# Performance work log

Hardware: AMD Instinct MI355X
Metric: run time of the kernel (lower is better)

Reference implementation:

```python
import jax, jax.numpy as jnp
import numpy as np

HEADS = 6
EPS = 1e-5


def _na_idx(L, k, d):
    # NATTEN-style dilated neighborhood: work within dilation cosets,
    # clamp window to stay inside the image (window shifts at borders).
    i = np.arange(L)
    g = i % d
    p = i // d
    Lg = (L - g + d - 1) // d  # coset length per position
    start = np.clip(p - k // 2, 0, Lg - k)
    j = np.arange(k)
    nbr = g[:, None] + d * (start[:, None] + j[None, :])          # [L,k] neighbor coords
    rel = (start[:, None] + j[None, :]) - p[:, None] + (k - 1)    # [L,k] rpb index in [0,2k-2]
    return jnp.asarray(nbr, jnp.int32), jnp.asarray(rel, jnp.int32)


def _na2d(x, qkv_w, qkv_b, proj_w, proj_b, rpb, heads, k, d):
    # x: [B,H,W,C] NHWC neighborhood attention with relative positional bias
    B, H, W, C = x.shape
    dh = C // heads
    scale = dh ** -0.5
    qkv = (x @ qkv_w + qkv_b).reshape(B, H, W, 3, heads, dh)
    qkv = jnp.transpose(qkv, (3, 0, 4, 1, 2, 5))  # [3,B,h,H,W,dh]
    q, kk, v = qkv[0] * scale, qkv[1], qkv[2]
    nh, rh = _na_idx(H, k, d)
    nw, rw = _na_idx(W, k, d)

    def gather(t):  # [B,h,H,W,dh] -> [B,h,H,W,k,k,dh]
        t = t[:, :, nh]              # [B,h,H,k,W,dh]
        t = t[:, :, :, :, nw]        # [B,h,H,k,W,k,dh]
        return jnp.transpose(t, (0, 1, 2, 4, 3, 5, 6))

    kn, vn = gather(kk), gather(v)
    attn = jnp.einsum('bhxyd,bhxyijd->bhxyij', q, kn)  # [B,h,H,W,k,k]
    bias = rpb[:, rh]                  # [h,H,k,2k-1]
    bias = bias[:, :, :, rw]           # [h,H,k,W,k]
    bias = jnp.transpose(bias, (0, 1, 3, 2, 4))  # [h,H,W,k,k]
    attn = attn + bias[None]
    attn = jax.nn.softmax(attn.reshape(B, heads, H, W, k * k), axis=-1)
    attn = attn.reshape(B, heads, H, W, k, k)
    out = jnp.einsum('bhxyij,bhxyijd->bhxyd', attn, vn)
    out = jnp.transpose(out, (0, 2, 3, 1, 4)).reshape(B, H, W, C)
    return out @ proj_w + proj_b


def _rln(x, w, b, m1_w, m1_b, m2_w, m2_b):
    # Revised LayerNorm: normalize over (C,H,W) per sample; meta1/meta2 are 1x1 convs on std/mean
    mean = jnp.mean(x, axis=(1, 2, 3), keepdims=True)
    std = jnp.sqrt(jnp.mean((x - mean) ** 2, axis=(1, 2, 3), keepdims=True) + EPS)
    out = (x - mean) / std * w + b
    rescale = m1_w[None, :, None, None] * std + m1_b[None, :, None, None]
    rebias = m2_w[None, :, None, None] * mean + m2_b[None, :, None, None]
    return out, rescale, rebias


def _c11(x, w, b):  # 1x1 conv on NCHW == per-pixel linear
    return jnp.einsum('bchw,oc->bohw', x, w) + b[None, :, None, None]


def _gelu(x):
    return jax.nn.gelu(x, approximate=False)


def reference(x, ln_w, ln_b, m1_w, m1_b, m2_w, m2_b, qkv1_w, qkv1_b, proj1_w, proj1_b, rpb1, qkv2_w, qkv2_b, proj2_w, proj2_b, rpb2, mlp_w1, mlp_b1, mlp_w2, mlp_b2, bn_g, bn_b, bn_m, bn_v, pa_w1, pa_b1, pa_w2, pa_b2, ca_w1, ca_b1, ca_w2, ca_b2, m2a_w1, m2a_b1, m2a_w2, m2a_b2):
    # ---- NA block 1 (kernel 7, dilation 1) ----
    sc = x
    y, rs, rb = _rln(x, ln_w, ln_b, m1_w, m1_b, m2_w, m2_b)
    a = _na2d(jnp.transpose(y, (0, 2, 3, 1)), qkv1_w, qkv1_b, proj1_w, proj1_b, rpb1, HEADS, 7, 1)
    x = sc + jnp.transpose(a, (0, 3, 1, 2)) * rs + rb
    # ---- NA block 2 (kernel 5, dilation 8) ----
    sc = x
    y, rs, rb = _rln(x, ln_w, ln_b, m1_w, m1_b, m2_w, m2_b)
    a = _na2d(jnp.transpose(y, (0, 2, 3, 1)), qkv2_w, qkv2_b, proj2_w, proj2_b, rpb2, HEADS, 5, 8)
    x = sc + jnp.transpose(a, (0, 3, 1, 2)) * rs + rb
    # ---- MLP (source reuses the pre-attn2 shortcut `sc`) ----
    y, rs, rb = _rln(x, ln_w, ln_b, m1_w, m1_b, m2_w, m2_b)
    m = _c11(jax.nn.relu(_c11(y, mlp_w1, mlp_b1)), mlp_w2, mlp_b2)
    x = sc + m * rs + rb
    # ---- BN + pixel attention + channel attention + mlp2 ----
    sc = x
    inv = jax.lax.rsqrt(bn_v + EPS)
    y = (x - bn_m[None, :, None, None]) * (inv * bn_g)[None, :, None, None] + bn_b[None, :, None, None]
    pa = jax.nn.sigmoid(_c11(_gelu(_c11(y, pa_w1, pa_b1)), pa_w2, pa_b2))  # [B,1,H,W]
    y = pa * y
    gap = jnp.mean(y, axis=(2, 3), keepdims=True)
    ca = jax.nn.sigmoid(_c11(_gelu(_c11(gap, ca_w1, ca_b1)), ca_w2, ca_b2))  # [B,C,1,1]
    y = ca * y
    y = _c11(_gelu(_c11(y, m2a_w1, m2a_b1)), m2a_w2, m2a_b2)
    return sc + y


def setup_inputs() -> dict:
    key = jax.random.key(0)
    B, C, H, W, HID = 4, 96, 64, 64, 384
    ks = iter(jax.random.split(key, 48))

    def rn(shape, s=0.02):
        return jax.random.normal(next(ks), shape, jnp.float32) * s

    d = {}
    d['x'] = jax.random.normal(next(ks), (B, C, H, W), jnp.float32)
    d['ln_w'] = jnp.ones((1, C, 1, 1), jnp.float32)
    d['ln_b'] = jnp.zeros((1, C, 1, 1), jnp.float32)
    d['m1_w'] = rn((C,)); d['m1_b'] = jnp.ones((C,), jnp.float32)
    d['m2_w'] = rn((C,)); d['m2_b'] = jnp.zeros((C,), jnp.float32)
    d['qkv1_w'] = rn((C, 3 * C)); d['qkv1_b'] = jnp.zeros((3 * C,), jnp.float32)
    d['proj1_w'] = rn((C, C)); d['proj1_b'] = jnp.zeros((C,), jnp.float32)
    d['rpb1'] = rn((HEADS, 13, 13))
    d['qkv2_w'] = rn((C, 3 * C)); d['qkv2_b'] = jnp.zeros((3 * C,), jnp.float32)
    d['proj2_w'] = rn((C, C)); d['proj2_b'] = jnp.zeros((C,), jnp.float32)
    d['rpb2'] = rn((HEADS, 9, 9))
    d['mlp_w1'] = rn((HID, C)); d['mlp_b1'] = jnp.zeros((HID,), jnp.float32)
    d['mlp_w2'] = rn((C, HID)); d['mlp_b2'] = jnp.zeros((C,), jnp.float32)
    d['bn_g'] = jnp.ones((C,), jnp.float32); d['bn_b'] = jnp.zeros((C,), jnp.float32)
    d['bn_m'] = jnp.zeros((C,), jnp.float32); d['bn_v'] = jnp.ones((C,), jnp.float32)
    d['pa_w1'] = rn((C // 8, C)); d['pa_b1'] = jnp.zeros((C // 8,), jnp.float32)
    d['pa_w2'] = rn((1, C // 8)); d['pa_b2'] = jnp.zeros((1,), jnp.float32)
    d['ca_w1'] = rn((C, C)); d['ca_b1'] = jnp.zeros((C,), jnp.float32)
    d['ca_w2'] = rn((C, C)); d['ca_b2'] = jnp.zeros((C,), jnp.float32)
    d['m2a_w1'] = rn((C, C)); d['m2a_b1'] = jnp.zeros((C,), jnp.float32)
    d['m2a_w2'] = rn((C, C)); d['m2a_b2'] = jnp.zeros((C,), jnp.float32)
    return d
```

## Files before the change

kernel.cpp:

```cpp
#include <hip/hip_runtime.h>
#include <math.h>

#define CC 96
#define NP 4096
#define NHEADS 6
#define NELEMF 393216.0f
#define EPSF 1e-5f

typedef __attribute__((ext_vector_type(8))) short bf16x8;
typedef __attribute__((ext_vector_type(4))) float f32x4;
#define MFMA16(a,b,c) __builtin_amdgcn_mfma_f32_16x16x32_bf16(a,b,c,0,0,0)

#define WQKV1  64
#define WQKV2  (WQKV1+13824)
#define WPROJ1 (WQKV2+13824)
#define WPROJ2 (WPROJ1+4608)
#define WMLP1  (WPROJ2+4608)
#define WMLP2  (WMLP1+18432)
#define WM2A1  (WMLP2+18432)
#define WM2A2  (WM2A1+4608)
#define WPA1T  (WM2A2+4608)
#define WBNS   (WPA1T+1152)
#define WS_Q   870784
#define WS_K   (WS_Q+786432)
#define WS_V   (WS_K+786432)
#define WS_ATTPM (WS_V+786432)
#define WS_X1  (WS_ATTPM+786432)
#define WS_X2  (WS_X1+1572864)
#define WS_X3  (WS_X2+1572864)
#define WS_PA  (WS_X3+1572864)
#define WS_GAP (WS_PA+16384)
#define WS_CA  (WS_GAP+384)

__device__ __forceinline__ float gelu_f(float x){
  return 0.5f * x * (1.0f + erff(x * 0.7071067811865476f));
}
__device__ __forceinline__ float sigmoid_f(float x){
  return 1.0f / (1.0f + __expf(-x));
}
__device__ __forceinline__ unsigned short bfr(float f){
  unsigned int u = __float_as_uint(f);
  u += 0x7fffu + ((u >> 16) & 1u);
  return (unsigned short)(u >> 16);
}
__device__ __forceinline__ float bflo(unsigned int u){ return __uint_as_float(u << 16); }
__device__ __forceinline__ float bfhi(unsigned int u){ return __uint_as_float(u & 0xffff0000u); }
__device__ __forceinline__ void get_ms(const float* st, int b, float& mean, float& inv, float& stdv){
  float s = st[b], s2 = st[4+b];
  mean = s * (1.0f/NELEMF);
  float var = fmaxf(s2 * (1.0f/NELEMF) - mean*mean, 0.0f);
  stdv = sqrtf(var + EPSF);
  inv = 1.0f / stdv;
}

__global__ void prep_stats_kernel(const float* __restrict__ x, float* __restrict__ st,
                             const float* __restrict__ q1, const float* __restrict__ q2,
                             const float* __restrict__ p1, const float* __restrict__ p2,
                             const float* __restrict__ w1, const float* __restrict__ w2,
                             const float* __restrict__ a1, const float* __restrict__ a2,
                             const float* __restrict__ pw1,
                             const float* __restrict__ bg, const float* __restrict__ bb,
                             const float* __restrict__ bm, const float* __restrict__ bv,
                             float* __restrict__ ws){
  if(blockIdx.x < 384){
    int b = blockIdx.x / CC, c = blockIdx.x % CC;
    const float* p = x + (b*CC + c)*NP;
    float s = 0.f, s2 = 0.f;
    for(int i = threadIdx.x; i < NP; i += 256){ float v = p[i]; s += v; s2 = fmaf(v, v, s2); }
    for(int off = 32; off > 0; off >>= 1){ s += __shfl_down(s, off); s2 += __shfl_down(s2, off); }
    __shared__ float ls[8];
    int wid = threadIdx.x >> 6;
    if((threadIdx.x & 63) == 0){ ls[wid] = s; ls[4+wid] = s2; }
    __syncthreads();
    if(threadIdx.x == 0){
      atomicAdd(&st[b],   ls[0]+ls[1]+ls[2]+ls[3]);
      atomicAdd(&st[4+b], ls[4]+ls[5]+ls[6]+ls[7]);
    }
    return;
  }
  int gid = (blockIdx.x - 384)*256 + threadIdx.x;
  if(gid < 27648){ int n = gid/96, c = gid%96; ((unsigned short*)(ws+WQKV1))[gid] = bfr(q1[c*288+n]); }
  else if(gid < 55296){ int g = gid-27648; int n = g/96, c = g%96; ((unsigned short*)(ws+WQKV2))[g] = bfr(q2[c*288+n]); }
  else if(gid < 64512){ int g = gid-55296; int n = g/96, c = g%96; ((unsigned short*)(ws+WPROJ1))[g] = bfr(p1[c*96+n]); }
  else if(gid < 73728){ int g = gid-64512; int n = g/96, c = g%96; ((unsigned short*)(ws+WPROJ2))[g] = bfr(p2[c*96+n]); }
  else if(gid < 110592){ int g = gid-73728; ((unsigned short*)(ws+WMLP1))[g] = bfr(w1[g]); }
  else if(gid < 147456){ int g = gid-110592; ((unsigned short*)(ws+WMLP2))[g] = bfr(w2[g]); }
  else if(gid < 156672){ int g = gid-147456; ((unsigned short*)(ws+WM2A1))[g] = bfr(a1[g]); }
  else if(gid < 165888){ int g = gid-156672; ((unsigned short*)(ws+WM2A2))[g] = bfr(a2[g]); }
  else if(gid < 167040){ int g = gid-165888; int c = g/12, h = g%12; ws[WPA1T + g] = pw1[h*96+c]; }
  else if(gid < 167136){ int c = gid-167040;
    float sc = rsqrtf(bv[c] + EPSF) * bg[c];
    ws[WBNS + c] = sc;
    ws[WBNS + 96 + c] = bb[c] - bm[c]*sc;
  }
}

__global__ void __launch_bounds__(256) gemm_qkv_kernel(
    const float* __restrict__ xin, const float* __restrict__ st,
    const float* __restrict__ lnw, const float* __restrict__ lnb,
    const unsigned short* __restrict__ wT, const float* __restrict__ qb,
    unsigned short* __restrict__ qo, unsigned short* __restrict__ ko, unsigned short* __restrict__ vo){
  __shared__ unsigned short Atl[64*104];
  __shared__ float scl[96], ofs[96];
  int m_base = blockIdx.x*64;
  int nh = blockIdx.y;
  int b = m_base >> 12, pxl0 = m_base & 4095;
  float mean, inv, stdv; get_ms(st, b, mean, inv, stdv);
  int tid = threadIdx.x;
  if(tid < 96){ float s = inv*lnw[tid]; scl[tid] = s; ofs[tid] = lnb[tid] - mean*s; }
  __syncthreads();
  const float* src = xin + (size_t)b*CC*NP + pxl0;
  for(int idx = tid; idx < 96*64; idx += 256){
    int c = idx >> 6, p = idx & 63;
    Atl[p*104 + c] = bfr(fmaf(src[c*NP + p], scl[c], ofs[c]));
  }
  __syncthreads();
  int w = tid >> 6, lane = tid & 63, ml = lane & 15, q = lane >> 4;
  const unsigned short* arow = Atl + (w*16 + ml)*104;
  bf16x8 av[3];
  #pragma unroll
  for(int ks = 0; ks < 3; ++ks) av[ks] = *(const bf16x8*)(arow + ks*32 + q*8);
  f32x4 z = {0.f,0.f,0.f,0.f};
  #pragma unroll
  for(int g = 0; g < 3; ++g){
    f32x4 acc[3] = {z, z, z};
    #pragma unroll
    for(int ks = 0; ks < 3; ++ks){
      #pragma unroll
      for(int gg = 0; gg < 3; ++gg){
        bf16x8 bv = *(const bf16x8*)(wT + (nh*144 + g*48 + gg*16 + ml)*96 + ks*32 + q*8);
        acc[gg] = MFMA16(av[ks], bv, acc[gg]);
      }
    }
    #pragma unroll
    for(int gg = 0; gg < 3; ++gg){
      int nfb = nh*144 + g*48 + gg*16;
      int t = nfb/96, head = (nfb%96) >> 4;
      float scale = (t == 0) ? 0.25f : 1.0f;
      unsigned short* dst = (t == 0) ? qo : (t == 1) ? ko : vo;
      float bias = qb[nfb + ml];
      #pragma unroll
      for(int r = 0; r < 4; ++r){
        int pxl = pxl0 + w*16 + q*4 + r;
        dst[(((size_t)(b*NHEADS + head))*NP + pxl)*16 + ml] = bfr((acc[gg][r] + bias)*scale);
      }
    }
  }
}

__global__ void __launch_bounds__(256) gemm_proj_kernel(
    const unsigned short* __restrict__ attpm, const unsigned short* __restrict__ wT,
    const float* __restrict__ pb, const float* __restrict__ scx, const float* __restrict__ st,
    const float* __restrict__ m1w, const float* __restrict__ m1b,
    const float* __restrict__ m2w, const float* __restrict__ m2b,
    float* __restrict__ dst, float* __restrict__ st_out){
  int w = threadIdx.x >> 6, lane = threadIdx.x & 63;
  int ml = lane & 15, q = lane >> 4;
  int m_base = blockIdx.x*128 + w*32;
  int n0 = blockIdx.y*48;
  f32x4 acc[2][3];
  f32x4 z = {0.f,0.f,0.f,0.f};
  #pragma unroll
  for(int f=0; f<2; ++f) for(int g=0; g<3; ++g) acc[f][g] = z;
  {
    const bf16x8* a0 = (const bf16x8*)(attpm + (size_t)(m_base + ml)*96 + q*8);
    const bf16x8* a1 = (const bf16x8*)(attpm + (size_t)(m_base + 16 + ml)*96 + q*8);
    #pragma unroll
    for(int ks = 0; ks < 3; ++ks){
      bf16x8 av0 = a0[ks*4], av1 = a1[ks*4];
      #pragma unroll
      for(int g = 0; g < 3; ++g){
        bf16x8 bv = *(const bf16x8*)(wT + (n0 + g*16 + ml)*96 + ks*32 + q*8);
        acc[0][g] = MFMA16(av0, bv, acc[0][g]);
        acc[1][g] = MFMA16(av1, bv, acc[1][g]);
      }
    }
  }
  __shared__ float T[48*133];
  #pragma unroll
  for(int f = 0; f < 2; ++f)
    #pragma unroll
    for(int g = 0; g < 3; ++g)
      #pragma unroll
      for(int r = 0; r < 4; ++r)
        T[(g*16 + ml)*133 + w*32 + f*16 + q*4 + r] = acc[f][g][r];
  __syncthreads();
  int b = (blockIdx.x*128) >> 12, pxl0 = (blockIdx.x*128) & 4095;
  float mean, inv, stdv; get_ms(st, b, mean, inv, stdv);
  float s = 0.f, s2 = 0.f;
  for(int idx = threadIdx.x; idx < 48*128; idx += 256){
    int row = idx >> 7, px = idx & 127;
    int n = n0 + row;
    float rsf = fmaf(m1w[n], stdv, m1b[n]);
    float rbf = fmaf(m2w[n], mean, m2b[n]);
    int ad = (b*CC + n)*NP + pxl0 + px;
    float val = scx[ad] + (T[row*133 + px] + pb[n])*rsf + rbf;
    dst[ad] = val;
    s += val; s2 = fmaf(val, val, s2);
  }
  for(int off = 32; off > 0; off >>= 1){ s += __shfl_down(s, off); s2 += __shfl_down(s2, off); }
  __shared__ float ls[8];
  int wid = threadIdx.x >> 6;
  if((threadIdx.x & 63) == 0){ ls[wid] = s; ls[4+wid] = s2; }
  __syncthreads();
  if(threadIdx.x == 0){
    atomicAdd(&st_out[b],   ls[0]+ls[1]+ls[2]+ls[3]);
    atomicAdd(&st_out[4+b], ls[4]+ls[5]+ls[6]+ls[7]);
  }
}

__global__ void __launch_bounds__(256) gemm_mlp1_kernel(
    const float* __restrict__ xin, const float* __restrict__ st,
    const float* __restrict__ lnw, const float* __restrict__ lnb,
    const unsigned short* __restrict__ wT, const float* __restrict__ b1,
    unsigned short* __restrict__ hid){
  __shared__ unsigned short Atl[64*104];
  __shared__ float scl[96], ofs[96];
  int m_base = blockIdx.x*64;
  int nh = blockIdx.y;
  int b = m_base >> 12, pxl0 = m_base & 4095;
  float mean, inv, stdv; get_ms(st, b, mean, inv, stdv);
  int tid = threadIdx.x;
  if(tid < 96){ float s = inv*lnw[tid]; scl[tid] = s; ofs[tid] = lnb[tid] - mean*s; }
  __syncthreads();
  const float* src = xin + (size_t)b*CC*NP + pxl0;
  for(int idx = tid; idx < 96*64; idx += 256){
    int c = idx >> 6, p = idx & 63;
    Atl[p*104 + c] = bfr(fmaf(src[c*NP + p], scl[c], ofs[c]));
  }
  __syncthreads();
  int w = tid >> 6, lane = tid & 63, ml = lane & 15, q = lane >> 4;
  const unsigned short* arow = Atl + (w*16 + ml)*104;
  bf16x8 av[3];
  #pragma unroll
  for(int ks = 0; ks < 3; ++ks) av[ks] = *(const bf16x8*)(arow + ks*32 + q*8);
  f32x4 z = {0.f,0.f,0.f,0.f};
  #pragma unroll
  for(int g = 0; g < 4; ++g){
    f32x4 acc[3] = {z, z, z};
    #pragma unroll
    for(int ks = 0; ks < 3; ++ks){
      #pragma unroll
      for(int gg = 0; gg < 3; ++gg){
        bf16x8 bv = *(const bf16x8*)(wT + (nh*192 + g*48 + gg*16 + ml)*96 + ks*32 + q*8);
        acc[gg] = MFMA16(av[ks], bv, acc[gg]);
      }
    }
    #pragma unroll
    for(int gg = 0; gg < 3; ++gg){
      int n = nh*192 + g*48 + gg*16 + ml;
      float bias = b1[n];
      #pragma unroll
      for(int r = 0; r < 4; ++r){
        int m = m_base + w*16 + q*4 + r;
        hid[(size_t)m*384 + n] = bfr(fmaxf(acc[gg][r] + bias, 0.f));
      }
    }
  }
}

__global__ void __launch_bounds__(256) gemm_mlp2_kernel(
    const unsigned short* __restrict__ hid, const unsigned short* __restrict__ wT,
    const float* __restrict__ b2, const float* __restrict__ scx, const float* __restrict__ st,
    const float* __restrict__ m1w, const float* __restrict__ m1b,
    const float* __restrict__ m2w, const float* __restrict__ m2b,
    float* __restrict__ dst){
  int w = threadIdx.x >> 6, lane = threadIdx.x & 63;
  int ml = lane & 15, q = lane >> 4;
  int m_base = blockIdx.x*128 + w*32;
  int n0 = blockIdx.y*48;
  f32x4 acc[2][3];
  f32x4 z = {0.f,0.f,0.f,0.f};
  #pragma unroll
  for(int f=0; f<2; ++f) for(int g=0; g<3; ++g) acc[f][g] = z;
  {
    const bf16x8* a0 = (const bf16x8*)(hid + (size_t)(m_base + ml)*384 + q*8);
    const bf16x8* a1 = (const bf16x8*)(hid + (size_t)(m_base + 16 + ml)*384 + q*8);
    #pragma unroll
    for(int ks = 0; ks < 12; ++ks){
      bf16x8 av0 = a0[ks*4], av1 = a1[ks*4];
      #pragma unroll
      for(int g = 0; g < 3; ++g){
        bf16x8 bv = *(const bf16x8*)(wT + (n0 + g*16 + ml)*384 + ks*32 + q*8);
        acc[0][g] = MFMA16(av0, bv, acc[0][g]);
        acc[1][g] = MFMA16(av1, bv, acc[1][g]);
      }
    }
  }
  __shared__ float T[48*133];
  #pragma unroll
  for(int f = 0; f < 2; ++f)
    #pragma unroll
    for(int g = 0; g < 3; ++g)
      #pragma unroll
      for(int r = 0; r < 4; ++r)
        T[(g*16 + ml)*133 + w*32 + f*16 + q*4 + r] = acc[f][g][r];
  __syncthreads();
  int b = (blockIdx.x*128) >> 12, pxl0 = (blockIdx.x*128) & 4095;
  float mean, inv, stdv; get_ms(st, b, mean, inv, stdv);
  for(int idx = threadIdx.x; idx < 48*128; idx += 256){
    int row = idx >> 7, px = idx & 127;
    int n = n0 + row;
    float rsf = fmaf(m1w[n], stdv, m1b[n]);
    float rbf = fmaf(m2w[n], mean, m2b[n]);
    int ad = (b*CC + n)*NP + pxl0 + px;
    dst[ad] = scx[ad] + (T[row*133 + px] + b2[n])*rsf + rbf;
  }
}

__global__ void __launch_bounds__(256) gemm_m2a_kernel(
    const float* __restrict__ x3, const float* __restrict__ bns,
    const float* __restrict__ pa, const float* __restrict__ ca,
    const unsigned short* __restrict__ w1T, const float* __restrict__ b1,
    const unsigned short* __restrict__ w2T, const float* __restrict__ b2,
    const float* __restrict__ scx, float* __restrict__ outp){
  __shared__ __align__(16) char smbuf[26624];
  __shared__ float scl[96], ofs[96], pal[64];
  unsigned short* Atl = (unsigned short*)smbuf;
  unsigned short* tl2 = (unsigned short*)(smbuf + 13312);
  float* T = (float*)smbuf;
  int m_base = blockIdx.x*64;
  int b = m_base >> 12, pxl0 = m_base & 4095;
  int tid = threadIdx.x;
  if(tid < 96){ float cv = ca[b*96 + tid]; scl[tid] = bns[tid]*cv; ofs[tid] = bns[96+tid]*cv; }
  if(tid >= 128 && tid < 192) pal[tid-128] = pa[m_base + (tid-128)];
  __syncthreads();
  const float* src = x3 + (size_t)b*CC*NP + pxl0;
  for(int idx = tid; idx < 96*64; idx += 256){
    int c = idx >> 6, p = idx & 63;
    Atl[p*104 + c] = bfr(fmaf(src[c*NP + p], scl[c], ofs[c]) * pal[p]);
  }
  __syncthreads();
  int w = tid >> 6, lane = tid & 63, ml = lane & 15, q = lane >> 4;
  f32x4 z = {0.f,0.f,0.f,0.f};
  f32x4 acc1[6];
  #pragma unroll
  for(int g=0; g<6; ++g) acc1[g] = z;
  {
    const unsigned short* arow = Atl + (w*16 + ml)*104;
    #pragma unroll
    for(int ks = 0; ks < 3; ++ks){
      bf16x8 av = *(const bf16x8*)(arow + ks*32 + q*8);
      #pragma unroll
      for(int g = 0; g < 6; ++g){
        bf16x8 bv = *(const bf16x8*)(w1T + (g*16 + ml)*96 + ks*32 + q*8);
        acc1[g] = MFMA16(av, bv, acc1[g]);
      }
    }
  }
  #pragma unroll
  for(int g = 0; g < 6; ++g){
    float bias = b1[g*16 + ml];
    #pragma unroll
    for(int r = 0; r < 4; ++r)
      tl2[(w*16 + q*4 + r)*104 + g*16 + ml] = bfr(gelu_f(acc1[g][r] + bias));
  }
  __syncthreads();
  f32x4 acc2[6];
  #pragma unroll
  for(int g=0; g<6; ++g) acc2[g] = z;
  {
    const unsigned short* arow = tl2 + (w*16 + ml)*104;
    #pragma unroll
    for(int ks = 0; ks < 3; ++ks){
      bf16x8 av = *(const bf16x8*)(arow + ks*32 + q*8);
      #pragma unroll
      for(int g = 0; g < 6; ++g){
        bf16x8 bv = *(const bf16x8*)(w2T + (g*16 + ml)*96 + ks*32 + q*8);
        acc2[g] = MFMA16(av, bv, acc2[g]);
      }
    }
  }
  __syncthreads();
  #pragma unroll
  for(int g = 0; g < 6; ++g)
    #pragma unroll
    for(int r = 0; r < 4; ++r)
      T[(g*16 + ml)*68 + w*16 + q*4 + r] = acc2[g][r];
  __syncthreads();
  for(int idx = tid; idx < 96*64; idx += 256){
    int n = idx >> 6, p = idx & 63;
    int ad = (b*CC + n)*NP + pxl0 + p;
    outp[ad] = scx[ad] + T[n*68 + p] + b2[n];
  }
}

template<int K, int D, int RPB>
__global__ void __launch_bounds__(256) attn_kernel(
    const unsigned short* __restrict__ qb, const unsigned short* __restrict__ kb,
    const unsigned short* __restrict__ vb, const float* __restrict__ rpb,
    unsigned short* __restrict__ outp){
  int bh = blockIdx.x >> 6;
  int x = blockIdx.x & 63;
  int head = bh % NHEADS, b = bh / NHEADS;

  int gx = x % D, px = x / D;
  int Lgx = (64 - gx + D - 1) / D;
  int sx = min(max(px - K/2, 0), Lgx - K);

  __shared__ unsigned int sm[2*K*512];
  unsigned int* kl = sm;
  unsigned int* vl = sm + K*512;
  const unsigned int* kg = (const unsigned int*)(kb + (size_t)bh*NP*16);
  const unsigned int* vg = (const unsigned int*)(vb + (size_t)bh*NP*16);
  int tid = threadIdx.x;
  #pragma unroll
  for(int i = 0; i < K; ++i){
    int hh = gx + D*(sx + i);
    ((uint2*)(kl + i*512))[tid] = ((const uint2*)(kg + hh*512))[tid];
    ((uint2*)(vl + i*512))[tid] = ((const uint2*)(vg + hh*512))[tid];
  }
  __syncthreads();

  int pixoff = tid >> 2, t = tid & 3;
  int y = pixoff;
  int pix = x*64 + y;
  uint2 qd = *(const uint2*)(qb + ((size_t)bh*NP + pix)*16 + 4*t);
  float qx = bflo(qd.x), qy = bfhi(qd.x), qz = bflo(qd.y), qw = bfhi(qd.y);

  int gy = y % D, py = y / D;
  int Lgy = (64 - gy + D - 1) / D;
  int sy = min(max(py - K/2, 0), Lgy - K);

  float sc[K*K];
  #pragma unroll
  for(int i = 0; i < K; ++i){
    #pragma unroll
    for(int j = 0; j < K; ++j){
      int ww = gy + D*(sy + j);
      uint2 kv = *(const uint2*)(kl + i*512 + ww*8 + t*2);
      float s = qx*bflo(kv.x);
      s = fmaf(qy, bfhi(kv.x), s);
      s = fmaf(qz, bflo(kv.y), s);
      s = fmaf(qw, bfhi(kv.y), s);
      sc[i*K + j] = s;
    }
  }
  float mx = -1e30f;
  #pragma unroll
  for(int i = 0; i < K; ++i){
    const float* brow = rpb + (head*RPB + (sx + i - px + (K-1)))*RPB + (sy - py + (K-1));
    #pragma unroll
    for(int j = 0; j < K; ++j){
      float s = sc[i*K + j];
      s += __shfl_xor(s, 1);
      s += __shfl_xor(s, 2);
      s += brow[j];
      sc[i*K + j] = s;
      mx = fmaxf(mx, s);
    }
  }
  float sum = 0.f;
  #pragma unroll
  for(int n = 0; n < K*K; ++n){ float e = __expf(sc[n] - mx); sc[n] = e; sum += e; }
  float rs = 1.0f / sum;
  float4 acc = {0,0,0,0};
  #pragma unroll
  for(int i = 0; i < K; ++i){
    #pragma unroll
    for(int j = 0; j < K; ++j){
      int ww = gy + D*(sy + j);
      float wgt = sc[i*K + j] * rs;
      uint2 vv = *(const uint2*)(vl + i*512 + ww*8 + t*2);
      acc.x = fmaf(wgt, bflo(vv.x), acc.x);
      acc.y = fmaf(wgt, bfhi(vv.x), acc.y);
      acc.z = fmaf(wgt, bflo(vv.y), acc.z);
      acc.w = fmaf(wgt, bfhi(vv.y), acc.w);
    }
  }
  ushort4 o4;
  o4.x = bfr(acc.x); o4.y = bfr(acc.y); o4.z = bfr(acc.z); o4.w = bfr(acc.w);
  *(ushort4*)(outp + ((size_t)(b*NP + pix))*96 + head*16 + 4*t) = o4;
}

__global__ void __launch_bounds__(256) pa_kernel(
    const float* __restrict__ x3, const float* __restrict__ bns,
    const float* __restrict__ w1t, const float* __restrict__ b1,
    const float* __restrict__ w2, const float* __restrict__ b2,
    float* __restrict__ pa){
  int b = blockIdx.x >> 6;
  int px0 = (blockIdx.x & 63)*64;
  int pxq = threadIdx.x >> 2, t = threadIdx.x & 3;
  int p = px0 + pxq;
  float acc[12];
  #pragma unroll
  for(int h = 0; h < 12; ++h) acc[h] = 0.f;
  #pragma unroll 6
  for(int cc = 0; cc < 24; ++cc){
    int c = t*24 + cc;
    float yv = fmaf(x3[(b*CC + c)*NP + p], bns[c], bns[96 + c]);
    #pragma unroll
    for(int h = 0; h < 12; ++h) acc[h] = fmaf(yv, w1t[c*12 + h], acc[h]);
  }
  #pragma unroll
  for(int h = 0; h < 12; ++h){
    acc[h] += __shfl_xor(acc[h], 1);
    acc[h] += __shfl_xor(acc[h], 2);
  }
  float s = b2[0];
  #pragma unroll
  for(int h = 0; h < 12; ++h) s = fmaf(gelu_f(acc[h] + b1[h]), w2[h], s);
  if(t == 0) pa[b*NP + p] = sigmoid_f(s);
}

__global__ void gap_kernel(const float* __restrict__ x3, const float* __restrict__ bns,
                           const float* __restrict__ pa, float* __restrict__ gap){
  int b = blockIdx.x / CC, c = blockIdx.x % CC;
  float scb = bns[c], shb = bns[96 + c];
  float s = 0.f;
  for(int i = threadIdx.x; i < NP; i += 256)
    s = fmaf(fmaf(x3[(b*CC + c)*NP + i], scb, shb), pa[b*NP + i], s);
  for(int off = 32; off > 0; off >>= 1) s += __shfl_down(s, off);
  __shared__ float ls[4];
  if((threadIdx.x & 63) == 0) ls[threadIdx.x >> 6] = s;
  __syncthreads();
  if(threadIdx.x == 0) gap[blockIdx.x] = (ls[0]+ls[1]+ls[2]+ls[3]) * (1.0f/4096.0f);
}

__global__ void ca_kernel(const float* __restrict__ gap, const float* __restrict__ w1,
                          const float* __restrict__ b1, const float* __restrict__ w2,
                          const float* __restrict__ b2, float* __restrict__ ca){
  int b = blockIdx.x; int o = threadIdx.x;
  __shared__ float g[96], t[96];
  if(o < 96) g[o] = gap[b*96 + o];
  __syncthreads();
  if(o < 96){
    float a = b1[o];
    for(int c = 0; c < 96; ++c) a = fmaf(g[c], w1[o*96 + c], a);
    t[o] = gelu_f(a);
  }
  __syncthreads();
  if(o < 96){
    float a = b2[o];
    for(int c = 0; c < 96; ++c) a = fmaf(t[c], w2[o*96 + c], a);
    ca[b*96 + o] = sigmoid_f(a);
  }
}

extern "C" void kernel_launch(void* const* d_in, const int* in_sizes, int n_in,
                              void* d_out, int out_size, void* d_ws, size_t ws_size,
                              hipStream_t stream){
  (void)in_sizes; (void)n_in; (void)out_size; (void)ws_size;
  const float* x     = (const float*)d_in[0];
  const float* lnw   = (const float*)d_in[1];
  const float* lnb   = (const float*)d_in[2];
  const float* m1w   = (const float*)d_in[3];
  const float* m1b   = (const float*)d_in[4];
  const float* m2w   = (const float*)d_in[5];
  const float* m2b   = (const float*)d_in[6];
  const float* qkv1w = (const float*)d_in[7];
  const float* qkv1b = (const float*)d_in[8];
  const float* proj1w= (const float*)d_in[9];
  const float* proj1b= (const float*)d_in[10];
  const float* rpb1  = (const float*)d_in[11];
  const float* qkv2w = (const float*)d_in[12];
  const float* qkv2b = (const float*)d_in[13];
  const float* proj2w= (const float*)d_in[14];
  const float* proj2b= (const float*)d_in[15];
  const float* rpb2  = (const float*)d_in[16];
  const float* mw1   = (const float*)d_in[17];
  const float* mb1   = (const float*)d_in[18];
  const float* mw2   = (const float*)d_in[19];
  const float* mb2   = (const float*)d_in[20];
  const float* bng   = (const float*)d_in[21];
  const float* bnb   = (const float*)d_in[22];
  const float* bnm   = (const float*)d_in[23];
  const float* bnv   = (const float*)d_in[24];
  const float* paw1  = (const float*)d_in[25];
  const float* pab1  = (const float*)d_in[26];
  const float* paw2  = (const float*)d_in[27];
  const float* pab2  = (const float*)d_in[28];
  const float* caw1  = (const float*)d_in[29];
  const float* cab1  = (const float*)d_in[30];
  const float* caw2  = (const float*)d_in[31];
  const float* cab2  = (const float*)d_in[32];
  const float* aw1   = (const float*)d_in[33];
  const float* ab1   = (const float*)d_in[34];
  const float* aw2   = (const float*)d_in[35];
  const float* ab2   = (const float*)d_in[36];

  float* ws  = (float*)d_ws;
  float* out = (float*)d_out;
  float* st0 = ws;
  float* st1 = ws + 8;
  float* st2 = ws + 16;
  unsigned short* q     = (unsigned short*)(ws + WS_Q);
  unsigned short* k     = (unsigned short*)(ws + WS_K);
  unsigned short* v     = (unsigned short*)(ws + WS_V);
  unsigned short* attpm = (unsigned short*)(ws + WS_ATTPM);
  unsigned short* hid   = (unsigned short*)(ws + WS_Q);
  float* x1  = ws + WS_X1;
  float* x2  = ws + WS_X2;
  float* x3  = ws + WS_X3;
  float* pab = ws + WS_PA;
  float* gpb = ws + WS_GAP;
  float* cab = ws + WS_CA;
  float* bns = ws + WBNS;

  hipMemsetAsync(d_ws, 0, 64*sizeof(float), stream);
  prep_stats_kernel<<<1040, 256, 0, stream>>>(x, st0, qkv1w, qkv2w, proj1w, proj2w,
                                              mw1, mw2, aw1, aw2, paw1,
                                              bng, bnb, bnm, bnv, ws);

  gemm_qkv_kernel<<<dim3(256,2), 256, 0, stream>>>(x, st0, lnw, lnb, (unsigned short*)(ws+WQKV1), qkv1b, q, k, v);
  attn_kernel<7,1,13><<<1536, 256, 0, stream>>>(q, k, v, rpb1, attpm);
  gemm_proj_kernel<<<dim3(128,2), 256, 0, stream>>>(attpm, (unsigned short*)(ws+WPROJ1), proj1b,
                                                    x, st0, m1w, m1b, m2w, m2b, x1, st1);

  gemm_qkv_kernel<<<dim3(256,2), 256, 0, stream>>>(x1, st1, lnw, lnb, (unsigned short*)(ws+WQKV2), qkv2b, q, k, v);
  attn_kernel<5,8,9><<<1536, 256, 0, stream>>>(q, k, v, rpb2, attpm);
  gemm_proj_kernel<<<dim3(128,2), 256, 0, stream>>>(attpm, (unsigned short*)(ws+WPROJ2), proj2b,
                                                    x1, st1, m1w, m1b, m2w, m2b, x2, st2);

  gemm_mlp1_kernel<<<dim3(256,2), 256, 0, stream>>>(x2, st2, lnw, lnb, (unsigned short*)(ws+WMLP1), mb1, hid);
  gemm_mlp2_kernel<<<dim3(128,2), 256, 0, stream>>>(hid, (unsigned short*)(ws+WMLP2), mb2,
                                                    x1, st2, m1w, m1b, m2w, m2b, x3);

  pa_kernel<<<256, 256, 0, stream>>>(x3, bns, ws + WPA1T, pab1, paw2, pab2, pab);
  gap_kernel<<<384, 256, 0, stream>>>(x3, bns, pab, gpb);
  ca_kernel<<<4, 128, 0, stream>>>(gpb, caw1, cab1, caw2, cab2, cab);
  gemm_m2a_kernel<<<256, 256, 0, stream>>>(x3, bns, pab, cab, (unsigned short*)(ws+WM2A1), ab1,
                                           (unsigned short*)(ws+WM2A2), ab2, x3, out);
}
```

Baseline: 300.6 us.

## Store intermediate residuals in bf16, vectorize tile loads, merge N-split GEMM blocks

The intermediate activations x1 and x2 are now stored as bf16 instead of fp32, which halves the global traffic for writes in the projection kernels and for reads in the later GEMMs. The A-tile staging loops in the qkv, mlp1 and m2a kernels load four pixels per thread with vector loads instead of scalar loads. The qkv and mlp1 kernels no longer split the output columns across two blocks in blockIdx.y, so each block computes all columns and the normalized input tile is loaded and normalized once rather than twice. This costs extra bf16 rounding error on the residual paths and halves the grid size of those two GEMMs, which lowers parallelism.

```diff
diff --git a/kernel.cpp b/kernel.cpp
--- a/kernel.cpp
+++ b/kernel.cpp
@@ -43,6 +43,7 @@
   u += 0x7fffu + ((u >> 16) & 1u);
   return (unsigned short)(u >> 16);
 }
+__device__ __forceinline__ float bflo16(unsigned short u){ return __uint_as_float(((unsigned int)u) << 16); }
 __device__ __forceinline__ float bflo(unsigned int u){ return __uint_as_float(u << 16); }
 __device__ __forceinline__ float bfhi(unsigned int u){ return __uint_as_float(u & 0xffff0000u); }
 __device__ __forceinline__ void get_ms(const float* st, int b, float& mean, float& inv, float& stdv){
@@ -51,6 +52,13 @@
   float var = fmaxf(s2 * (1.0f/NELEMF) - mean*mean, 0.0f);
   stdv = sqrtf(var + EPSF);
   inv = 1.0f / stdv;
+}
+__device__ __forceinline__ float ldf(const float* p, int i){ return p[i]; }
+__device__ __forceinline__ float ldf(const unsigned short* p, int i){ return bflo16(p[i]); }
+__device__ __forceinline__ void load4(const float* p, float4& v){ v = *(const float4*)p; }
+__device__ __forceinline__ void load4(const unsigned short* p, float4& v){
+  ushort4 u = *(const ushort4*)p;
+  v.x = bflo16(u.x); v.y = bflo16(u.y); v.z = bflo16(u.z); v.w = bflo16(u.w);
 }
 
 __global__ void prep_stats_kernel(const float* __restrict__ x, float* __restrict__ st,
@@ -95,24 +103,29 @@
   }
 }
 
+template<typename AT>
 __global__ void __launch_bounds__(256) gemm_qkv_kernel(
-    const float* __restrict__ xin, const float* __restrict__ st,
+    const AT* __restrict__ xin, const float* __restrict__ st,
     const float* __restrict__ lnw, const float* __restrict__ lnb,
     const unsigned short* __restrict__ wT, const float* __restrict__ qb,
     unsigned short* __restrict__ qo, unsigned short* __restrict__ ko, unsigned short* __restrict__ vo){
   __shared__ unsigned short Atl[64*104];
   __shared__ float scl[96], ofs[96];
   int m_base = blockIdx.x*64;
-  int nh = blockIdx.y;
   int b = m_base >> 12, pxl0 = m_base & 4095;
   float mean, inv, stdv; get_ms(st, b, mean, inv, stdv);
   int tid = threadIdx.x;
   if(tid < 96){ float s = inv*lnw[tid]; scl[tid] = s; ofs[tid] = lnb[tid] - mean*s; }
   __syncthreads();
-  const float* src = xin + (size_t)b*CC*NP + pxl0;
-  for(int idx = tid; idx < 96*64; idx += 256){
-    int c = idx >> 6, p = idx & 63;
-    Atl[p*104 + c] = bfr(fmaf(src[c*NP + p], scl[c], ofs[c]));
+  const AT* src = xin + (size_t)b*CC*NP + pxl0;
+  for(int idx = tid; idx < 96*16; idx += 256){
+    int c = idx >> 4, p4 = (idx & 15) << 2;
+    float4 v; load4(src + (size_t)c*NP + p4, v);
+    float s = scl[c], o = ofs[c];
+    Atl[(p4+0)*104 + c] = bfr(fmaf(v.x, s, o));
+    Atl[(p4+1)*104 + c] = bfr(fmaf(v.y, s, o));
+    Atl[(p4+2)*104 + c] = bfr(fmaf(v.z, s, o));
+    Atl[(p4+3)*104 + c] = bfr(fmaf(v.w, s, o));
   }
   __syncthreads();
   int w = tid >> 6, lane = tid & 63, ml = lane & 15, q = lane >> 4;
@@ -122,19 +135,19 @@
   for(int ks = 0; ks < 3; ++ks) av[ks] = *(const bf16x8*)(arow + ks*32 + q*8);
   f32x4 z = {0.f,0.f,0.f,0.f};
   #pragma unroll
-  for(int g = 0; g < 3; ++g){
+  for(int g = 0; g < 6; ++g){
     f32x4 acc[3] = {z, z, z};
     #pragma unroll
     for(int ks = 0; ks < 3; ++ks){
       #pragma unroll
       for(int gg = 0; gg < 3; ++gg){
-        bf16x8 bv = *(const bf16x8*)(wT + (nh*144 + g*48 + gg*16 + ml)*96 + ks*32 + q*8);
+        bf16x8 bv = *(const bf16x8*)(wT + (g*48 + gg*16 + ml)*96 + ks*32 + q*8);
         acc[gg] = MFMA16(av[ks], bv, acc[gg]);
       }
     }
     #pragma unroll
     for(int gg = 0; gg < 3; ++gg){
-      int nfb = nh*144 + g*48 + gg*16;
+      int nfb = g*48 + gg*16;
       int t = nfb/96, head = (nfb%96) >> 4;
       float scale = (t == 0) ? 0.25f : 1.0f;
       unsigned short* dst = (t == 0) ? qo : (t == 1) ? ko : vo;
@@ -148,12 +161,13 @@
   }
 }
 
+template<typename SCT>
 __global__ void __launch_bounds__(256) gemm_proj_kernel(
     const unsigned short* __restrict__ attpm, const unsigned short* __restrict__ wT,
-    const float* __restrict__ pb, const float* __restrict__ scx, const float* __restrict__ st,
+    const float* __restrict__ pb, const SCT* __restrict__ scx, const float* __restrict__ st,
     const float* __restrict__ m1w, const float* __restrict__ m1b,
     const float* __restrict__ m2w, const float* __restrict__ m2b,
-    float* __restrict__ dst, float* __restrict__ st_out){
+    unsigned short* __restrict__ dst, float* __restrict__ st_out){
   int w = threadIdx.x >> 6, lane = threadIdx.x & 63;
   int ml = lane & 15, q = lane >> 4;
   int m_base = blockIdx.x*128 + w*32;
@@ -194,8 +208,8 @@
     float rsf = fmaf(m1w[n], stdv, m1b[n]);
     float rbf = fmaf(m2w[n], mean, m2b[n]);
     int ad = (b*CC + n)*NP + pxl0 + px;
-    float val = scx[ad] + (T[row*133 + px] + pb[n])*rsf + rbf;
-    dst[ad] = val;
+    float val = ldf(scx, ad) + (T[row*133 + px] + pb[n])*rsf + rbf;
+    dst[ad] = bfr(val);
     s += val; s2 = fmaf(val, val, s2);
   }
   for(int off = 32; off > 0; off >>= 1){ s += __shfl_down(s, off); s2 += __shfl_down(s2, off); }
@@ -210,23 +224,27 @@
 }
 
 __global__ void __launch_bounds__(256) gemm_mlp1_kernel(
-    const float* __restrict__ xin, const float* __restrict__ st,
+    const unsigned short* __restrict__ xin, const float* __restrict__ st,
     const float* __restrict__ lnw, const float* __restrict__ lnb,
     const unsigned short* __restrict__ wT, const float* __restrict__ b1,
     unsigned short* __restrict__ hid){
   __shared__ unsigned short Atl[64*104];
   __shared__ float scl[96], ofs[96];
   int m_base = blockIdx.x*64;
-  int nh = blockIdx.y;
   int b = m_base >> 12, pxl0 = m_base & 4095;
   float mean, inv, stdv; get_ms(st, b, mean, inv, stdv);
   int tid = threadIdx.x;
   if(tid < 96){ float s = inv*lnw[tid]; scl[tid] = s; ofs[tid] = lnb[tid] - mean*s; }
   __syncthreads();
-  const float* src = xin + (size_t)b*CC*NP + pxl0;
-  for(int idx = tid; idx < 96*64; idx += 256){
-    int c = idx >> 6, p = idx & 63;
-    Atl[p*104 + c] = bfr(fmaf(src[c*NP + p], scl[c], ofs[c]));
+  const unsigned short* src = xin + (size_t)b*CC*NP + pxl0;
+  for(int idx = tid; idx < 96*16; idx += 256){
+    int c = idx >> 4, p4 = (idx & 15) << 2;
+    float4 v; load4(src + (size_t)c*NP + p4, v);
+    float s = scl[c], o = ofs[c];
+    Atl[(p4+0)*104 + c] = bfr(fmaf(v.x, s, o));
+    Atl[(p4+1)*104 + c] = bfr(fmaf(v.y, s, o));
+    Atl[(p4+2)*104 + c] = bfr(fmaf(v.z, s, o));
+    Atl[(p4+3)*104 + c] = bfr(fmaf(v.w, s, o));
   }
   __syncthreads();
   int w = tid >> 6, lane = tid & 63, ml = lane & 15, q = lane >> 4;
@@ -236,19 +254,19 @@
   for(int ks = 0; ks < 3; ++ks) av[ks] = *(const bf16x8*)(arow + ks*32 + q*8);
   f32x4 z = {0.f,0.f,0.f,0.f};
   #pragma unroll
-  for(int g = 0; g < 4; ++g){
+  for(int g = 0; g < 8; ++g){
     f32x4 acc[3] = {z, z, z};
     #pragma unroll
     for(int ks = 0; ks < 3; ++ks){
       #pragma unroll
       for(int gg = 0; gg < 3; ++gg){
-        bf16x8 bv = *(const bf16x8*)(wT + (nh*192 + g*48 + gg*16 + ml)*96 + ks*32 + q*8);
+        bf16x8 bv = *(const bf16x8*)(wT + (g*48 + gg*16 + ml)*96 + ks*32 + q*8);
         acc[gg] = MFMA16(av[ks], bv, acc[gg]);
       }
     }
     #pragma unroll
     for(int gg = 0; gg < 3; ++gg){
-      int n = nh*192 + g*48 + gg*16 + ml;
+      int n = g*48 + gg*16 + ml;
       float bias = b1[n];
       #pragma unroll
       for(int r = 0; r < 4; ++r){
@@ -261,7 +279,7 @@
 
 __global__ void __launch_bounds__(256) gemm_mlp2_kernel(
     const unsigned short* __restrict__ hid, const unsigned short* __restrict__ wT,
-    const float* __restrict__ b2, const float* __restrict__ scx, const float* __restrict__ st,
+    const float* __restrict__ b2, const unsigned short* __restrict__ scx, const float* __restrict__ st,
     const float* __restrict__ m1w, const float* __restrict__ m1b,
     const float* __restrict__ m2w, const float* __restrict__ m2b,
     float* __restrict__ dst){
@@ -304,7 +322,7 @@
     float rsf = fmaf(m1w[n], stdv, m1b[n]);
     float rbf = fmaf(m2w[n], mean, m2b[n]);
     int ad = (b*CC + n)*NP + pxl0 + px;
-    dst[ad] = scx[ad] + (T[row*133 + px] + b2[n])*rsf + rbf;
+    dst[ad] = ldf(scx, ad) + (T[row*133 + px] + b2[n])*rsf + rbf;
   }
 }
 
@@ -326,9 +344,14 @@
   if(tid >= 128 && tid < 192) pal[tid-128] = pa[m_base + (tid-128)];
   __syncthreads();
   const float* src = x3 + (size_t)b*CC*NP + pxl0;
-  for(int idx = tid; idx < 96*64; idx += 256){
-    int c = idx >> 6, p = idx & 63;
-    Atl[p*104 + c] = bfr(fmaf(src[c*NP + p], scl[c], ofs[c]) * pal[p]);
+  for(int idx = tid; idx < 96*16; idx += 256){
+    int c = idx >> 4, p4 = (idx & 15) << 2;
+    float4 v = *(const float4*)(src + (size_t)c*NP + p4);
+    float s = scl[c], o = ofs[c];
+    Atl[(p4+0)*104 + c] = bfr(fmaf(v.x, s, o) * pal[p4+0]);
+    Atl[(p4+1)*104 + c] = bfr(fmaf(v.y, s, o) * pal[p4+1]);
+    Atl[(p4+2)*104 + c] = bfr(fmaf(v.z, s, o) * pal[p4+2]);
+    Atl[(p4+3)*104 + c] = bfr(fmaf(v.w, s, o) * pal[p4+3]);
   }
   __syncthreads();
   int w = tid >> 6, lane = tid & 63, ml = lane & 15, q = lane >> 4;
@@ -589,8 +612,8 @@
   unsigned short* v     = (unsigned short*)(ws + WS_V);
   unsigned short* attpm = (unsigned short*)(ws + WS_ATTPM);
   unsigned short* hid   = (unsigned short*)(ws + WS_Q);
-  float* x1  = ws + WS_X1;
-  float* x2  = ws + WS_X2;
+  unsigned short* x1b   = (unsigned short*)(ws + WS_X1);
+  unsigned short* x2b   = (unsigned short*)(ws + WS_X2);
   float* x3  = ws + WS_X3;
   float* pab = ws + WS_PA;
   float* gpb = ws + WS_GAP;
@@ -602,19 +625,22 @@
                                               mw1, mw2, aw1, aw2, paw1,
                                               bng, bnb, bnm, bnv, ws);
 
-  gemm_qkv_kernel<<<dim3(256,2), 256, 0, stream>>>(x, st0, lnw, lnb, (unsigned short*)(ws+WQKV1), qkv1b, q, k, v);
+  gemm_qkv_kernel<float><<<256, 256, 0, stream>>>(x, st0, lnw, lnb,
+      (unsigned short*)(ws+WQKV1), qkv1b, q, k, v);
   attn_kernel<7,1,13><<<1536, 256, 0, stream>>>(q, k, v, rpb1, attpm);
-  gemm_proj_kernel<<<dim3(128,2), 256, 0, stream>>>(attpm, (unsigned short*)(ws+WPROJ1), proj1b,
-                                                    x, st0, m1w, m1b, m2w, m2b, x1, st1);
-
-  gemm_qkv_kernel<<<dim3(256,2), 256, 0, stream>>>(x1, st1, lnw, lnb, (unsigned short*)(ws+WQKV2), qkv2b, q, k, v);
+  gemm_proj_kernel<float><<<dim3(128,2), 256, 0, stream>>>(attpm, (unsigned short*)(ws+WPROJ1),
+      proj1b, x, st0, m1w, m1b, m2w, m2b, x1b, st1);
+
+  gemm_qkv_kernel<unsigned short><<<256, 256, 0, stream>>>(x1b, st1, lnw, lnb,
+      (unsigned short*)(ws+WQKV2), qkv2b, q, k, v);
   attn_kernel<5,8,9><<<1536, 256, 0, stream>>>(q, k, v, rpb2, attpm);
-  gemm_proj_kernel<<<dim3(128,2), 256, 0, stream>>>(attpm, (unsigned short*)(ws+WPROJ2), proj2b,
-                                                    x1, st1, m1w, m1b, m2w, m2b, x2, st2);
-
-  gemm_mlp1_kernel<<<dim3(256,2), 256, 0, stream>>>(x2, st2, lnw, lnb, (unsigned short*)(ws+WMLP1), mb1, hid);
+  gemm_proj_kernel<unsigned short><<<dim3(128,2), 256, 0, stream>>>(attpm, (unsigned short*)(ws+WPROJ2),
+      proj2b, x1b, st1, m1w, m1b, m2w, m2b, x2b, st2);
+
+  gemm_mlp1_kernel<<<256, 256, 0, stream>>>(x2b, st2, lnw, lnb,
+      (unsigned short*)(ws+WMLP1), mb1, hid);
   gemm_mlp2_kernel<<<dim3(128,2), 256, 0, stream>>>(hid, (unsigned short*)(ws+WMLP2), mb2,
-                                                    x1, st2, m1w, m1b, m2w, m2b, x3);
+      x1b, st2, m1w, m1b, m2w, m2b, x3);
 
   pa_kernel<<<256, 256, 0, stream>>>(x3, bns, ws + WPA1T, pab1, paw2, pab2, pab);
   gap_kernel<<<384, 256, 0, stream>>>(x3, bns, pab, gpb);
```

Measured after the change: 294.0 us. 1.02x faster.
